# Kernel tuning notes

Hardware: AMD Instinct MI355X
Metric: run time of the kernel (lower is better)

The kernel has to match this reference:

```python
import jax, jax.numpy as jnp
import numpy as np

OUT = 7        # RoIAlign output_size
SR = 2         # sampling_ratio
SCALE = 1.0 / 32.0


def roi_align(feat, boxes):
    """Torchvision-style RoIAlign (aligned=False) for a single image.
    feat: [C,H,W]; boxes: [N,4] xyxy in image coords. Returns [N,C,OUT,OUT]."""
    C, H, W = feat.shape
    b = boxes * SCALE
    x1, y1, x2, y2 = b[:, 0], b[:, 1], b[:, 2], b[:, 3]
    rw = jnp.maximum(x2 - x1, 1.0)
    rh = jnp.maximum(y2 - y1, 1.0)
    bw = rw / OUT  # bin width
    bh = rh / OUT  # bin height
    P = OUT * SR   # 14 sample points per axis
    i = jnp.arange(P)
    bin_idx = (i // SR).astype(feat.dtype)
    sub_idx = (i % SR).astype(feat.dtype)
    # sample coords: start + bin*binsize + (s+0.5)*binsize/SR  -> [N,P]
    ox = x1[:, None] + bin_idx[None, :] * bw[:, None] + (sub_idx[None, :] + 0.5) * (bw[:, None] / SR)
    oy = y1[:, None] + bin_idx[None, :] * bh[:, None] + (sub_idx[None, :] + 0.5) * (bh[:, None] / SR)

    def axis_terms(o, L):
        valid = (o >= -1.0) & (o <= float(L))
        oc = jnp.clip(o, 0.0, L - 1.0)
        i0 = jnp.floor(oc).astype(jnp.int32)
        i1 = jnp.minimum(i0 + 1, L - 1)
        l = oc - i0.astype(oc.dtype)
        return valid, i0, i1, l

    vy, y0, y1i, ly = axis_terms(oy, H)
    vx, x0, x1i, lx = axis_terms(ox, W)
    valid = (vy[:, :, None] & vx[:, None, :]).astype(feat.dtype)  # [N,P,P]

    def gather(yi, xi):  # -> [C,N,P,P]
        return feat[:, yi[:, :, None], xi[:, None, :]]

    wy0, wy1 = (1.0 - ly), ly
    wx0, wx1 = (1.0 - lx), lx
    val = (gather(y0, x0) * (wy0[:, :, None] * wx0[:, None, :])
           + gather(y0, x1i) * (wy0[:, :, None] * wx1[:, None, :])
           + gather(y1i, x0) * (wy1[:, :, None] * wx0[:, None, :])
           + gather(y1i, x1i) * (wy1[:, :, None] * wx1[:, None, :]))
    val = val * valid[None]                      # zero out-of-bounds samples
    val = jnp.transpose(val, (1, 0, 2, 3))       # [N,C,P,P]
    N = boxes.shape[0]
    val = val.reshape(N, C, OUT, SR, OUT, SR)
    return val.mean(axis=(3, 5))                 # average sampling points


def reference(feats1, feats2, proposals, W1, b1, W2, b2):
    N = proposals.shape[0]
    f1 = roi_align(feats1[0], proposals).reshape(N, -1)  # [N, C*49]
    f2 = roi_align(feats2[0], proposals).reshape(N, -1)
    feats_cat = jnp.concatenate([f1, f2], axis=1)        # [N, 2*C*49]
    h = jax.nn.relu(feats_cat @ W1 + b1)
    out = h @ W2 + b2                                    # [N, 11]
    obj_scores = jax.nn.sigmoid(out[:, :2])
    boxes = out[:, 2:10].reshape(-1, 2, 4)
    id_scores = jax.nn.sigmoid(out[:, 10])
    return (obj_scores[:, 0], obj_scores[:, 1], boxes[:, 0], boxes[:, 1], id_scores)


def setup_inputs() -> dict:
    key = jax.random.key(0)
    ks = jax.random.split(key, 8)
    C, H, W = 256, 32, 32
    N = 1024
    IMG = 1024.0
    feats1 = jax.random.normal(ks[0], (1, C, H, W), dtype=jnp.float32)
    feats2 = jax.random.normal(ks[1], (1, C, H, W), dtype=jnp.float32)
    # valid xyxy boxes in image coords
    cx = jax.random.uniform(ks[2], (N,), minval=0.0, maxval=IMG)
    cy = jax.random.uniform(ks[3], (N,), minval=0.0, maxval=IMG)
    hw = jax.random.uniform(ks[4], (N, 2), minval=16.0, maxval=160.0)
    x1 = jnp.clip(cx - hw[:, 0], 0.0, IMG - 2.0)
    y1 = jnp.clip(cy - hw[:, 1], 0.0, IMG - 2.0)
    x2 = jnp.clip(cx + hw[:, 0], x1 + 1.0, IMG)
    y2 = jnp.clip(cy + hw[:, 1], y1 + 1.0, IMG)
    proposals = jnp.stack([x1, y1, x2, y2], axis=1).astype(jnp.float32)
    d_in = 2 * C * OUT * OUT  # 25088
    W1 = jax.random.normal(ks[5], (d_in, 512), dtype=jnp.float32) * 0.02
    b1 = jnp.zeros((512,), dtype=jnp.float32)
    W2 = jax.random.normal(ks[6], (512, 11), dtype=jnp.float32) * 0.02
    b2 = jnp.zeros((11,), dtype=jnp.float32)
    return {"feats1": feats1, "feats2": feats2, "proposals": proposals,
            "W1": W1, "b1": b1, "W2": W2, "b2": b2}
```

## Files before the change

kernel.cpp:

```cpp
#include <hip/hip_runtime.h>
#include <hip/hip_bf16.h>

#define KTOT   25088
#define HALF_K 12544
#define HID    512
#define SPLITK 14
#define KCHUNK (KTOT/SPLITK)
#define NTILE  28

typedef __attribute__((ext_vector_type(8))) short short8;
typedef __attribute__((ext_vector_type(4))) float f32x4;

__device__ __forceinline__ unsigned short f2bf(float x) {
  __hip_bfloat16 h = __float2bfloat16(x);
  return *reinterpret_cast<unsigned short*>(&h);
}
__device__ __forceinline__ float bf2f(unsigned short u) {
  return __uint_as_float((unsigned)u << 16);
}

__global__ __launch_bounds__(256) void k_tfeat(const float* __restrict__ f1,
                                               const float* __restrict__ f2,
                                               __hip_bfloat16* __restrict__ ft) {
  __shared__ float tile[64][65];
  const int ct = blockIdx.x, yxt = blockIdx.y, map = blockIdx.z;
  const float* src = map ? f2 : f1;
  const int t = threadIdx.x, t4 = t >> 6, tl = t & 63;
#pragma unroll
  for (int pass = 0; pass < 16; ++pass) {
    int cl = pass * 4 + t4;
    tile[cl][tl] = src[(ct * 64 + cl) * 1024 + yxt * 64 + tl];
  }
  __syncthreads();
#pragma unroll
  for (int pass = 0; pass < 16; ++pass) {
    int yl = pass * 4 + t4;
    ft[(size_t)map * 262144 + (size_t)(yxt * 64 + yl) * 256 + ct * 64 + tl] =
        __float2bfloat16(tile[tl][yl]);
  }
}

__global__ __launch_bounds__(256) void k_tw1(const float* __restrict__ W1,
                                             __hip_bfloat16* __restrict__ W1t) {
  __shared__ float tile[64][65];
  const int ct = blockIdx.x & 3, jt = blockIdx.x >> 2;
  const int p = blockIdx.y, map = blockIdx.z;
  const int t = threadIdx.x, t4 = t >> 6, tl = t & 63;
#pragma unroll
  for (int pass = 0; pass < 16; ++pass) {
    int cl = pass * 4 + t4;
    int c = ct * 64 + cl;
    size_t krow = (size_t)map * HALF_K + (size_t)c * 49 + p;
    tile[cl][tl] = W1[krow * HID + jt * 64 + tl];
  }
  __syncthreads();
#pragma unroll
  for (int pass = 0; pass < 16; ++pass) {
    int jl = pass * 4 + t4;
    int j = jt * 64 + jl;
    W1t[(size_t)j * KTOT + (size_t)map * HALF_K + p * 256 + ct * 64 + tl] =
        __float2bfloat16(tile[tl][jl]);
  }
}

__global__ __launch_bounds__(256) void k_roi(const __hip_bfloat16* __restrict__ ft,
                                             const float* __restrict__ props,
                                             __hip_bfloat16* __restrict__ A) {
  __shared__ int   s_ny[4];
  __shared__ int   s_yoff[4][4];
  __shared__ float s_wy[4][4];
  __shared__ int   s_nx[4][7];
  __shared__ int   s_xoff[4][7][4];
  __shared__ float s_wx[4][7][4];
  const int t = threadIdx.x;
  const int nb = blockIdx.x * 4;
  const int oy = blockIdx.y;
  const float sc = 1.0f / 32.0f;
  if (t < 32) {
    const int b = t >> 3, j = t & 7;
    const int n = nb + b;
    float bx1 = props[n * 4 + 0] * sc, by1 = props[n * 4 + 1] * sc;
    float bx2 = props[n * 4 + 2] * sc, by2 = props[n * 4 + 3] * sc;
    float bw = fmaxf(bx2 - bx1, 1.f) * (1.f / 7.f);
    float bh = fmaxf(by2 - by1, 1.f) * (1.f / 7.f);
    const bool isY = (j == 0);
    const int i = isY ? oy : (j - 1);
    const float start = isY ? by1 : bx1;
    const float bs = isY ? bh : bw;
    int idxs[4]; float ws[4];
#pragma unroll
    for (int ssub = 0; ssub < 2; ++ssub) {
      float o = start + (float)i * bs + ((float)ssub + 0.5f) * bs * 0.5f;
      float v = (o >= -1.f && o <= 32.f) ? 1.f : 0.f;
      float oc = fminf(fmaxf(o, 0.f), 31.f);
      int i0 = (int)oc;
      int i1 = min(i0 + 1, 31);
      float l = oc - (float)i0;
      idxs[ssub * 2 + 0] = i0; ws[ssub * 2 + 0] = v * (1.f - l);
      idxs[ssub * 2 + 1] = i1; ws[ssub * 2 + 1] = v * l;
    }
    int mi[4]; float mw[4]; int cnt = 0;
#pragma unroll
    for (int e = 0; e < 4; ++e) {
      if (ws[e] != 0.f) {
        bool found = false;
#pragma unroll
        for (int f = 0; f < 4; ++f)
          if (f < cnt && mi[f] == idxs[e]) { mw[f] += ws[e]; found = true; }
        if (!found) { mi[cnt] = idxs[e]; mw[cnt] = ws[e]; ++cnt; }
      }
    }
#pragma unroll
    for (int f = 0; f < 4; ++f) if (f >= cnt) { mi[f] = 0; mw[f] = 0.f; }
    if (isY) {
      s_ny[b] = cnt;
#pragma unroll
      for (int f = 0; f < 4; ++f) { s_yoff[b][f] = mi[f] * 16384; s_wy[b][f] = mw[f] * 0.25f; }
    } else {
      s_nx[b][j - 1] = cnt;
#pragma unroll
      for (int f = 0; f < 4; ++f) { s_xoff[b][j - 1][f] = mi[f] * 512; s_wx[b][j - 1][f] = mw[f]; }
    }
  }
  __syncthreads();
  const int b = t >> 6, map = (t >> 5) & 1, q = t & 31;
  const char* fb = (const char*)ft;
  const unsigned qoff = (unsigned)(map * 524288 + q * 16);
  const int n = nb + b;
  const int ny = s_ny[b];
  unsigned ybase[4]; float wyr[4];
#pragma unroll
  for (int yy = 0; yy < 4; ++yy) {
    ybase[yy] = qoff + (unsigned)s_yoff[b][yy];
    wyr[yy] = s_wy[b][yy];
  }
  __hip_bfloat16* outp = A + (size_t)n * KTOT + map * HALF_K + q * 8 + oy * 7 * 256;
  for (int bl = 0; bl < 7; ++bl) {
    const int nx = s_nx[b][bl];
    float a[8] = {0.f, 0.f, 0.f, 0.f, 0.f, 0.f, 0.f, 0.f};
    for (int xx = 0; xx < nx; ++xx) {
      const unsigned xo = (unsigned)s_xoff[b][bl][xx];
      const float wxv = s_wx[b][bl][xx];
      for (int yy = 0; yy < ny; ++yy) {
        short8 u = *(const short8*)(fb + (ybase[yy] + xo));
        float w = wyr[yy] * wxv;
#pragma unroll
        for (int e = 0; e < 8; ++e) a[e] += w * bf2f((unsigned short)u[e]);
      }
    }
    short8 o;
#pragma unroll
    for (int e = 0; e < 8; ++e) o[e] = (short)f2bf(a[e]);
    *(short8*)(outp + bl * 256) = o;
  }
}

__device__ __forceinline__ void gl_lds16(const __hip_bfloat16* g, __hip_bfloat16* l) {
  __builtin_amdgcn_global_load_lds((const __attribute__((address_space(1))) void*)g,
                                   (__attribute__((address_space(3))) void*)l, 16, 0, 0);
}

__global__ __launch_bounds__(256, 2) void k_gemm1(const __hip_bfloat16* __restrict__ A,
                                                  const __hip_bfloat16* __restrict__ Bt,
                                                  unsigned short* __restrict__ parts, int M) {
  __shared__ __align__(16) __hip_bfloat16 As[2][128 * 64];
  __shared__ __align__(16) __hip_bfloat16 Bs[2][128 * 64];
  const int t = threadIdx.x;
  const int bid = blockIdx.x;
  const int newid = (bid & 7) * 56 + (bid >> 3);
  const int tile = newid & 31, kc = newid >> 5;
  const int row0 = (tile >> 2) * 128, col0 = (tile & 3) * 128;
  const size_t k0 = (size_t)kc * KCHUNK;

  const int srow = t >> 3;
  const int sq = (t & 7) ^ (srow & 7);
  const __hip_bfloat16* ags = A  + (size_t)(row0 + srow) * KTOT + k0 + sq * 8;
  const __hip_bfloat16* bgs = Bt + (size_t)(col0 + srow) * KTOT + k0 + sq * 8;

  const int lane = t & 63, wid = t >> 6;
  const int wm = wid >> 1, wn = wid & 1;
  const int r = lane & 15, g = lane >> 4;
  const int qs0 = ((g ^ (r & 7)) * 16);
  const int qs1 = qs0 ^ 64;
  const char* aB = (const char*)&As[0][0] + (wm * 64 + r) * 128;
  const char* bB = (const char*)&Bs[0][0] + (wn * 64 + r) * 128;

  f32x4 acc[4][4];
#pragma unroll
  for (int m = 0; m < 4; ++m)
#pragma unroll
    for (int n = 0; n < 4; ++n) acc[m][n] = (f32x4){0.f, 0.f, 0.f, 0.f};

#define STAGE(KT, BUF) do {                                             \
    const __hip_bfloat16* a_ = ags + (size_t)(KT) * 64;                 \
    const __hip_bfloat16* b_ = bgs + (size_t)(KT) * 64;                 \
    _Pragma("unroll")                                                   \
    for (int i_ = 0; i_ < 4; ++i_) {                                    \
      gl_lds16(a_ + (size_t)i_ * 32 * KTOT, &As[BUF][t * 8 + i_ * 2048]); \
      gl_lds16(b_ + (size_t)i_ * 32 * KTOT, &Bs[BUF][t * 8 + i_ * 2048]); \
    } } while (0)

#define TILE(BUF) do { const int bo_ = (BUF) * 16384;                   \
    short8 a0[4], b0[4], a1[4], b1[4];                                  \
    _Pragma("unroll")                                                   \
    for (int m_ = 0; m_ < 4; ++m_) {                                    \
      a0[m_] = *(const short8*)(aB + bo_ + m_ * 2048 + qs0);            \
      b0[m_] = *(const short8*)(bB + bo_ + m_ * 2048 + qs0);            \
    }                                                                   \
    _Pragma("unroll")                                                   \
    for (int m_ = 0; m_ < 4; ++m_) {                                    \
      a1[m_] = *(const short8*)(aB + bo_ + m_ * 2048 + qs1);            \
      b1[m_] = *(const short8*)(bB + bo_ + m_ * 2048 + qs1);            \
    }                                                                   \
    asm volatile("s_waitcnt lgkmcnt(8)" ::: "memory");                  \
    __builtin_amdgcn_sched_barrier(0);                                  \
    __builtin_amdgcn_s_setprio(1);                                      \
    _Pragma("unroll")                                                   \
    for (int m_ = 0; m_ < 4; ++m_) { _Pragma("unroll")                  \
      for (int n_ = 0; n_ < 4; ++n_)                                    \
        acc[m_][n_] = __builtin_amdgcn_mfma_f32_16x16x32_bf16(          \
            a0[m_], b0[n_], acc[m_][n_], 0, 0, 0); }                    \
    __builtin_amdgcn_s_setprio(0);                                      \
    asm volatile("s_waitcnt lgkmcnt(0)" ::: "memory");                  \
    __builtin_amdgcn_sched_barrier(0);                                  \
    __builtin_amdgcn_s_setprio(1);                                      \
    _Pragma("unroll")                                                   \
    for (int m_ = 0; m_ < 4; ++m_) { _Pragma("unroll")                  \
      for (int n_ = 0; n_ < 4; ++n_)                                    \
        acc[m_][n_] = __builtin_amdgcn_mfma_f32_16x16x32_bf16(          \
            a1[m_], b1[n_], acc[m_][n_], 0, 0, 0); }                    \
    __builtin_amdgcn_s_setprio(0);                                      \
  } while (0)

#define SB0 __builtin_amdgcn_sched_barrier(0)

  STAGE(0, 0);
  STAGE(1, 1);
  for (int kt = 0; kt < NTILE - 1; ++kt) {
    asm volatile("s_waitcnt vmcnt(8)" ::: "memory"); SB0;
    __builtin_amdgcn_s_barrier(); SB0;
    TILE(kt & 1);
    SB0;
    if (kt < NTILE - 2) {
      __builtin_amdgcn_s_barrier(); SB0;
      STAGE(kt + 2, kt & 1);
    }
  }
  asm volatile("s_waitcnt vmcnt(0)" ::: "memory"); SB0;
  __builtin_amdgcn_s_barrier(); SB0;
  TILE(1);

#undef STAGE
#undef TILE
#undef SB0

  unsigned short* P = parts + (size_t)kc * ((size_t)M * HID);
#pragma unroll
  for (int m = 0; m < 4; ++m)
#pragma unroll
    for (int n = 0; n < 4; ++n)
#pragma unroll
      for (int q = 0; q < 4; ++q) {
        int rr = row0 + wm * 64 + m * 16 + g * 4 + q;
        int cc = col0 + wn * 64 + n * 16 + r;
        P[(size_t)rr * HID + cc] = f2bf(acc[m][n][q]);
      }
}

__global__ __launch_bounds__(256) void k_head(const unsigned short* __restrict__ parts,
                                              const float* __restrict__ b1,
                                              const float* __restrict__ W2,
                                              const float* __restrict__ b2,
                                              float* __restrict__ out, int N) {
  __shared__ float hrow[512];
  __shared__ float part[16][17];
  const int n = blockIdx.x, t = threadIdx.x;
  if (t < 64) {
    float a[8] = {0.f, 0.f, 0.f, 0.f, 0.f, 0.f, 0.f, 0.f};
    const unsigned short* base = parts + (size_t)n * HID + t * 8;
    for (int p = 0; p < SPLITK; ++p) {
      short8 v = *(const short8*)(base + (size_t)p * ((size_t)N * HID));
#pragma unroll
      for (int e = 0; e < 8; ++e) a[e] += bf2f((unsigned short)v[e]);
    }
#pragma unroll
    for (int e = 0; e < 8; ++e) hrow[t * 8 + e] = fmaxf(a[e] + b1[t * 8 + e], 0.f);
  }
  __syncthreads();
  int j = t & 15, kc = t >> 4;
  float a = 0.f;
  if (j < 11) {
#pragma unroll
    for (int kk = 0; kk < 32; ++kk) {
      int k = kc * 32 + kk;
      a += hrow[k] * W2[k * 11 + j];
    }
  }
  part[kc][j] = a;
  __syncthreads();
  if (t < 11) {
    float sm = b2[t];
#pragma unroll
    for (int k2 = 0; k2 < 16; ++k2) sm += part[k2][t];
    if (t == 0)      out[n] = 1.f / (1.f + expf(-sm));
    else if (t == 1) out[N + n] = 1.f / (1.f + expf(-sm));
    else if (t < 6)  out[2 * N + n * 4 + (t - 2)] = sm;
    else if (t < 10) out[6 * N + n * 4 + (t - 6)] = sm;
    else             out[10 * N + n] = 1.f / (1.f + expf(-sm));
  }
}

extern "C" void kernel_launch(void* const* d_in, const int* in_sizes, int n_in,
                              void* d_out, int out_size, void* d_ws, size_t ws_size,
                              hipStream_t stream) {
  const float* feats1 = (const float*)d_in[0];
  const float* feats2 = (const float*)d_in[1];
  const float* props  = (const float*)d_in[2];
  const float* W1     = (const float*)d_in[3];
  const float* b1     = (const float*)d_in[4];
  const float* W2     = (const float*)d_in[5];
  const float* b2     = (const float*)d_in[6];
  float* out = (float*)d_out;
  const int N = in_sizes[2] / 4;

  char* ws = (char*)d_ws;
  __hip_bfloat16* ft = (__hip_bfloat16*)ws;
  __hip_bfloat16* Abuf = (__hip_bfloat16*)(ws + (1u << 20));
  size_t offW1t = (1u << 20) + (size_t)N * KTOT * 2;
  __hip_bfloat16* W1t = (__hip_bfloat16*)(ws + offW1t);
  size_t offParts = offW1t + (size_t)HID * KTOT * 2;
  unsigned short* parts = (unsigned short*)(ws + offParts);

  k_tfeat<<<dim3(4, 16, 2), 256, 0, stream>>>(feats1, feats2, ft);
  k_tw1<<<dim3(32, 49, 2), 256, 0, stream>>>(W1, W1t);
  k_roi<<<dim3(N / 4, 7), 256, 0, stream>>>(ft, props, Abuf);
  k_gemm1<<<dim3(32 * SPLITK), 256, 0, stream>>>(Abuf, W1t, parts, N);
  k_head<<<dim3(N), 256, 0, stream>>>(parts, b1, W2, b2, out, N);
}
```

Baseline: 83.01 us.

## Stage 64-channel feature slices in LDS for RoIAlign and unroll 3x3 taps

The feature map is re-laid out as 8 channel slices of 1024x64 bf16. Each RoIAlign block copies one 128KB slice into LDS with global_load_lds and then handles 32 boxes over all 7x7 bins, instead of gathering from global memory. The bilinear taps are deduplicated to at most 3 per axis and fully unrolled into 9 LDS loads per bin. The aim is to cut global gather traffic and the loop and launch overhead of the old per-row grid. In exchange the launch has only 256 blocks, and the large LDS footprint limits occupancy to about one block per CU.

```diff
diff --git a/kernel.cpp b/kernel.cpp
--- a/kernel.cpp
+++ b/kernel.cpp
@@ -19,9 +19,14 @@
   return __uint_as_float((unsigned)u << 16);
 }
 
+__device__ __forceinline__ void gl_lds16(const __hip_bfloat16* g, __hip_bfloat16* l) {
+  __builtin_amdgcn_global_load_lds((const __attribute__((address_space(1))) void*)g,
+                                   (__attribute__((address_space(3))) void*)l, 16, 0, 0);
+}
+
 __global__ __launch_bounds__(256) void k_tfeat(const float* __restrict__ f1,
                                                const float* __restrict__ f2,
-                                               __hip_bfloat16* __restrict__ ft) {
+                                               __hip_bfloat16* __restrict__ fts) {
   __shared__ float tile[64][65];
   const int ct = blockIdx.x, yxt = blockIdx.y, map = blockIdx.z;
   const float* src = map ? f2 : f1;
@@ -35,7 +40,7 @@
 #pragma unroll
   for (int pass = 0; pass < 16; ++pass) {
     int yl = pass * 4 + t4;
-    ft[(size_t)map * 262144 + (size_t)(yxt * 64 + yl) * 256 + ct * 64 + tl] =
+    fts[((size_t)(map * 4 + ct) * 1024 + yxt * 64 + yl) * 64 + tl] =
         __float2bfloat16(tile[tl][yl]);
   }
 }
@@ -63,28 +68,34 @@
   }
 }
 
-__global__ __launch_bounds__(256) void k_roi(const __hip_bfloat16* __restrict__ ft,
+__global__ __launch_bounds__(256) void k_roi(const __hip_bfloat16* __restrict__ fts,
                                              const float* __restrict__ props,
                                              __hip_bfloat16* __restrict__ A) {
-  __shared__ int   s_ny[4];
-  __shared__ int   s_yoff[4][4];
-  __shared__ float s_wy[4][4];
-  __shared__ int   s_nx[4][7];
-  __shared__ int   s_xoff[4][7][4];
-  __shared__ float s_wx[4][7][4];
+  __shared__ __align__(16) __hip_bfloat16 feat[1024 * 64];
+  __shared__ int   s_yoff[32][7][3];
+  __shared__ float s_wy[32][7][3];
+  __shared__ int   s_xoff[32][7][3];
+  __shared__ float s_wx[32][7][3];
   const int t = threadIdx.x;
-  const int nb = blockIdx.x * 4;
-  const int oy = blockIdx.y;
+  const int slice = blockIdx.x & 7;
+  const int grp = blockIdx.x >> 3;
+  {
+    const __hip_bfloat16* src = fts + (size_t)slice * 65536 + t * 8;
+    __hip_bfloat16* dst = &feat[t * 8];
+#pragma unroll
+    for (int i = 0; i < 32; ++i)
+      gl_lds16(src + i * 2048, dst + i * 2048);
+  }
   const float sc = 1.0f / 32.0f;
-  if (t < 32) {
-    const int b = t >> 3, j = t & 7;
-    const int n = nb + b;
+  for (int j = t; j < 448; j += 256) {
+    const int b = j / 14, ax = j % 14;
+    const int n = grp * 32 + b;
     float bx1 = props[n * 4 + 0] * sc, by1 = props[n * 4 + 1] * sc;
     float bx2 = props[n * 4 + 2] * sc, by2 = props[n * 4 + 3] * sc;
     float bw = fmaxf(bx2 - bx1, 1.f) * (1.f / 7.f);
     float bh = fmaxf(by2 - by1, 1.f) * (1.f / 7.f);
-    const bool isY = (j == 0);
-    const int i = isY ? oy : (j - 1);
+    const bool isY = (ax < 7);
+    const int i = isY ? ax : (ax - 7);
     const float start = isY ? by1 : bx1;
     const float bs = isY ? bh : bw;
     int idxs[4]; float ws[4];
@@ -99,65 +110,70 @@
       idxs[ssub * 2 + 0] = i0; ws[ssub * 2 + 0] = v * (1.f - l);
       idxs[ssub * 2 + 1] = i1; ws[ssub * 2 + 1] = v * l;
     }
-    int mi[4]; float mw[4]; int cnt = 0;
+    int mi[3] = {0, 0, 0}; float mw[3] = {0.f, 0.f, 0.f}; int cnt = 0;
 #pragma unroll
     for (int e = 0; e < 4; ++e) {
       if (ws[e] != 0.f) {
         bool found = false;
 #pragma unroll
-        for (int f = 0; f < 4; ++f)
+        for (int f = 0; f < 3; ++f)
           if (f < cnt && mi[f] == idxs[e]) { mw[f] += ws[e]; found = true; }
-        if (!found) { mi[cnt] = idxs[e]; mw[cnt] = ws[e]; ++cnt; }
+        if (!found && cnt < 3) { mi[cnt] = idxs[e]; mw[cnt] = ws[e]; ++cnt; }
       }
     }
-#pragma unroll
-    for (int f = 0; f < 4; ++f) if (f >= cnt) { mi[f] = 0; mw[f] = 0.f; }
     if (isY) {
-      s_ny[b] = cnt;
-#pragma unroll
-      for (int f = 0; f < 4; ++f) { s_yoff[b][f] = mi[f] * 16384; s_wy[b][f] = mw[f] * 0.25f; }
+#pragma unroll
+      for (int f = 0; f < 3; ++f) { s_yoff[b][i][f] = mi[f] * 4096; s_wy[b][i][f] = mw[f] * 0.25f; }
     } else {
-      s_nx[b][j - 1] = cnt;
-#pragma unroll
-      for (int f = 0; f < 4; ++f) { s_xoff[b][j - 1][f] = mi[f] * 512; s_wx[b][j - 1][f] = mw[f]; }
-    }
-  }
-  __syncthreads();
-  const int b = t >> 6, map = (t >> 5) & 1, q = t & 31;
-  const char* fb = (const char*)ft;
-  const unsigned qoff = (unsigned)(map * 524288 + q * 16);
-  const int n = nb + b;
-  const int ny = s_ny[b];
-  unsigned ybase[4]; float wyr[4];
-#pragma unroll
-  for (int yy = 0; yy < 4; ++yy) {
-    ybase[yy] = qoff + (unsigned)s_yoff[b][yy];
-    wyr[yy] = s_wy[b][yy];
-  }
-  __hip_bfloat16* outp = A + (size_t)n * KTOT + map * HALF_K + q * 8 + oy * 7 * 256;
-  for (int bl = 0; bl < 7; ++bl) {
-    const int nx = s_nx[b][bl];
-    float a[8] = {0.f, 0.f, 0.f, 0.f, 0.f, 0.f, 0.f, 0.f};
-    for (int xx = 0; xx < nx; ++xx) {
-      const unsigned xo = (unsigned)s_xoff[b][bl][xx];
-      const float wxv = s_wx[b][bl][xx];
-      for (int yy = 0; yy < ny; ++yy) {
-        short8 u = *(const short8*)(fb + (ybase[yy] + xo));
-        float w = wyr[yy] * wxv;
-#pragma unroll
-        for (int e = 0; e < 8; ++e) a[e] += w * bf2f((unsigned short)u[e]);
+#pragma unroll
+      for (int f = 0; f < 3; ++f) { s_xoff[b][i][f] = mi[f] * 128; s_wx[b][i][f] = mw[f]; }
+    }
+  }
+  __syncthreads();
+  const int b = t >> 3, cg = t & 7;
+  const int map = slice >> 2, c0 = (slice & 3) * 64;
+  const int n = grp * 32 + b;
+  const char* fb = (const char*)feat + cg * 16;
+  unsigned short* outp = (unsigned short*)A + (size_t)n * KTOT + map * HALF_K + c0 + cg * 8;
+  for (int oy = 0; oy < 7; ++oy) {
+    int yo0 = s_yoff[b][oy][0], yo1 = s_yoff[b][oy][1], yo2 = s_yoff[b][oy][2];
+    float wy0 = s_wy[b][oy][0], wy1 = s_wy[b][oy][1], wy2 = s_wy[b][oy][2];
+#pragma unroll
+    for (int ox = 0; ox < 7; ++ox) {
+      int xo0 = s_xoff[b][ox][0], xo1 = s_xoff[b][ox][1], xo2 = s_xoff[b][ox][2];
+      float wx0 = s_wx[b][ox][0], wx1 = s_wx[b][ox][1], wx2 = s_wx[b][ox][2];
+      short8 u00 = *(const short8*)(fb + yo0 + xo0);
+      short8 u01 = *(const short8*)(fb + yo0 + xo1);
+      short8 u02 = *(const short8*)(fb + yo0 + xo2);
+      short8 u10 = *(const short8*)(fb + yo1 + xo0);
+      short8 u11 = *(const short8*)(fb + yo1 + xo1);
+      short8 u12 = *(const short8*)(fb + yo1 + xo2);
+      short8 u20 = *(const short8*)(fb + yo2 + xo0);
+      short8 u21 = *(const short8*)(fb + yo2 + xo1);
+      short8 u22 = *(const short8*)(fb + yo2 + xo2);
+      float w00 = wy0 * wx0, w01 = wy0 * wx1, w02 = wy0 * wx2;
+      float w10 = wy1 * wx0, w11 = wy1 * wx1, w12 = wy1 * wx2;
+      float w20 = wy2 * wx0, w21 = wy2 * wx1, w22 = wy2 * wx2;
+      float a[8];
+#pragma unroll
+      for (int e = 0; e < 8; ++e) {
+        float s = w00 * bf2f((unsigned short)u00[e]);
+        s += w01 * bf2f((unsigned short)u01[e]);
+        s += w02 * bf2f((unsigned short)u02[e]);
+        s += w10 * bf2f((unsigned short)u10[e]);
+        s += w11 * bf2f((unsigned short)u11[e]);
+        s += w12 * bf2f((unsigned short)u12[e]);
+        s += w20 * bf2f((unsigned short)u20[e]);
+        s += w21 * bf2f((unsigned short)u21[e]);
+        s += w22 * bf2f((unsigned short)u22[e]);
+        a[e] = s;
       }
-    }
-    short8 o;
-#pragma unroll
-    for (int e = 0; e < 8; ++e) o[e] = (short)f2bf(a[e]);
-    *(short8*)(outp + bl * 256) = o;
-  }
-}
-
-__device__ __forceinline__ void gl_lds16(const __hip_bfloat16* g, __hip_bfloat16* l) {
-  __builtin_amdgcn_global_load_lds((const __attribute__((address_space(1))) void*)g,
-                                   (__attribute__((address_space(3))) void*)l, 16, 0, 0);
+      short8 o;
+#pragma unroll
+      for (int e = 0; e < 8; ++e) o[e] = (short)f2bf(a[e]);
+      *(short8*)(outp + (oy * 7 + ox) * 256) = o;
+    }
+  }
 }
 
 __global__ __launch_bounds__(256, 2) void k_gemm1(const __hip_bfloat16* __restrict__ A,
@@ -324,16 +340,16 @@
   const int N = in_sizes[2] / 4;
 
   char* ws = (char*)d_ws;
-  __hip_bfloat16* ft = (__hip_bfloat16*)ws;
+  __hip_bfloat16* fts = (__hip_bfloat16*)ws;
   __hip_bfloat16* Abuf = (__hip_bfloat16*)(ws + (1u << 20));
   size_t offW1t = (1u << 20) + (size_t)N * KTOT * 2;
   __hip_bfloat16* W1t = (__hip_bfloat16*)(ws + offW1t);
   size_t offParts = offW1t + (size_t)HID * KTOT * 2;
   unsigned short* parts = (unsigned short*)(ws + offParts);
 
-  k_tfeat<<<dim3(4, 16, 2), 256, 0, stream>>>(feats1, feats2, ft);
+  k_tfeat<<<dim3(4, 16, 2), 256, 0, stream>>>(feats1, feats2, fts);
   k_tw1<<<dim3(32, 49, 2), 256, 0, stream>>>(W1, W1t);
-  k_roi<<<dim3(N / 4, 7), 256, 0, stream>>>(ft, props, Abuf);
+  k_roi<<<dim3(256), 256, 0, stream>>>(fts, props, Abuf);
   k_gemm1<<<dim3(32 * SPLITK), 256, 0, stream>>>(Abuf, W1t, parts, N);
   k_head<<<dim3(N), 256, 0, stream>>>(parts, b1, W2, b2, out, N);
 }
```

Measured after the change: 81.12 us. 1.02x faster.
